# Optimization experiments

Measured on AMD Instinct MI355X. Metric: run time of the kernel, lower is better.

The kernel has to match this reference:

```python
import jax, jax.numpy as jnp
import numpy as np
import math

DIM = 768
HIDDEN = 3072
HEADS = 8
DEPTH = DIM // HEADS
EPS = 1e-5


def gelu_tanh(x):
    c = math.sqrt(2.0 / math.pi)
    return x * 0.5 * (1.0 + jnp.tanh(c * (x + 0.044715 * jnp.power(x, 3))))


def layer_norm(x, g, b):
    mu = jnp.mean(x, axis=-1, keepdims=True)
    var = jnp.mean(jnp.square(x - mu), axis=-1, keepdims=True)
    return (x - mu) * jax.lax.rsqrt(var + EPS) * g + b


def setup_inputs() -> dict:
    key = jax.random.key(0)
    ks = jax.random.split(key, 12)
    B, F, N = 2, 64, 128
    s = 0.02
    return {
        "q": jax.random.normal(ks[0], (B, F, N, DIM), jnp.float32),
        "k": jax.random.normal(ks[1], (B, F, N, DIM), jnp.float32),
        "v": jax.random.normal(ks[2], (B, F, N, DIM), jnp.float32),
        "ln1_g": jnp.ones((DIM,), jnp.float32),
        "ln1_b": jnp.zeros((DIM,), jnp.float32),
        "wq": jax.random.normal(ks[3], (DIM, DIM), jnp.float32) * s,
        "wk": jax.random.normal(ks[4], (DIM, DIM), jnp.float32) * s,
        "wv": jax.random.normal(ks[5], (DIM, DIM), jnp.float32) * s,
        "wo": jax.random.normal(ks[6], (DIM, DIM), jnp.float32) * s,
        "wo_b": jnp.zeros((DIM,), jnp.float32),
        "ln2_g": jnp.ones((DIM,), jnp.float32),
        "ln2_b": jnp.zeros((DIM,), jnp.float32),
        "w1": jax.random.normal(ks[7], (DIM, HIDDEN), jnp.float32) * s,
        "b1": jnp.zeros((HIDDEN,), jnp.float32),
        "w2": jax.random.normal(ks[8], (HIDDEN, DIM), jnp.float32) * s,
        "b2": jnpp if False else jnp.zeros((DIM,), jnp.float32),
    }


def reference(q, k, v, ln1_g, ln1_b, wq, wk, wv, wo, wo_b, ln2_g, ln2_b, w1, b1, w2, b2):
    # Shared norm1 applied to q, k, v (same params, as in the original)
    qn = layer_norm(q, ln1_g, ln1_b)
    kn = layer_norm(k, ln1_g, ln1_b)
    vn = layer_norm(v, ln1_g, ln1_b)

    B, F, N, _ = qn.shape
    # Projections (no bias on wq/wk/wv since att_bias=False)
    def split_heads(x):
        return x.reshape(B, F, N, HEADS, DEPTH).transpose(0, 1, 3, 2, 4)  # b f h n d

    qh = split_heads(qn @ wq)
    kh = split_heads(kn @ wk)
    vh = split_heads(vn @ wv)

    scale = DEPTH ** (-0.5)
    dots = jnp.einsum('bfhid,bfhjd->bfhij', qh, kh) * scale
    att_weight = jax.nn.softmax(dots, axis=-1)
    out = jnp.einsum('bfhij,bfhjd->bfhid', att_weight, vh)
    out = out.transpose(0, 1, 3, 2, 4).reshape(B, F, N, DIM)
    y = out @ wo + wo_b

    y = y + qn  # residual with normed q
    h = gelu_tanh(layer_norm(y, ln2_g, ln2_b) @ w1 + b1)
    out2 = h @ w2 + b2
    return out2 + y, att_weight
```

## Files before the change

kernel.cpp:

```cpp
#include <hip/hip_runtime.h>


#define NROWS 16384
#define TDIM 768
#define THID 3072
#define EPS 1e-5f

typedef short bf16x8 __attribute__((ext_vector_type(8)));
typedef float f32x4 __attribute__((ext_vector_type(4)));

__device__ __forceinline__ float b2f(unsigned short u) {
    union { unsigned int i; float f; } v; v.i = ((unsigned int)u) << 16; return v.f;
}
__device__ __forceinline__ unsigned short f2b(float f) {
    union { float f; unsigned int i; } v; v.f = f;
    unsigned int r = v.i + 0x7fffu + ((v.i >> 16) & 1u);
    return (unsigned short)(r >> 16);
}

__device__ __forceinline__ void async_copy16(const unsigned short* g, unsigned short* l) {
    __builtin_amdgcn_global_load_lds(
        (const __attribute__((address_space(1))) unsigned int*)g,
        (__attribute__((address_space(3))) unsigned int*)l,
        16, 0, 0);
}

__global__ __launch_bounds__(256) void cvt_t_kernel(
    const float* __restrict__ src, unsigned short* __restrict__ dst, int K, int N)
{
    __shared__ unsigned short tile[32][33];
    int n0 = blockIdx.x * 32, k0 = blockIdx.y * 32;
    int tx = threadIdx.x & 31, ty = threadIdx.x >> 5;
#pragma unroll
    for (int r = ty; r < 32; r += 8)
        tile[r][tx] = f2b(src[(size_t)(k0 + r) * N + n0 + tx]);
    __syncthreads();
#pragma unroll
    for (int r = ty; r < 32; r += 8)
        dst[(size_t)(n0 + r) * K + k0 + tx] = tile[tx][r];
}

template<bool IN_F32>
__global__ __launch_bounds__(256) void ln_kernel(
    const void* __restrict__ x0, const void* __restrict__ x1,
    const void* __restrict__ x2,
    const float* __restrict__ g, const float* __restrict__ bb,
    unsigned short* __restrict__ o0, unsigned short* __restrict__ o1,
    unsigned short* __restrict__ o2)
{
    int t = blockIdx.y;
    const void* x = (t == 0) ? x0 : (t == 1) ? x1 : x2;
    unsigned short* o = (t == 0) ? o0 : (t == 1) ? o1 : o2;
    size_t base = (size_t)blockIdx.x * TDIM;
    int tid = threadIdx.x;
    float v[3]; float sum = 0.f, sq = 0.f;
#pragma unroll
    for (int i = 0; i < 3; i++) {
        if constexpr (IN_F32) v[i] = ((const float*)x)[base + tid + i * 256];
        else v[i] = b2f(((const unsigned short*)x)[base + tid + i * 256]);
        sum += v[i]; sq += v[i] * v[i];
    }
#pragma unroll
    for (int o_ = 32; o_ > 0; o_ >>= 1) {
        sum += __shfl_down(sum, o_); sq += __shfl_down(sq, o_);
    }
    __shared__ float s1[4], s2[4];
    __shared__ float smu, srs;
    int wave = tid >> 6, lane = tid & 63;
    if (lane == 0) { s1[wave] = sum; s2[wave] = sq; }
    __syncthreads();
    if (tid == 0) {
        float S = s1[0] + s1[1] + s1[2] + s1[3];
        float Q = s2[0] + s2[1] + s2[2] + s2[3];
        float mu = S / (float)TDIM;
        float var = Q / (float)TDIM - mu * mu;
        smu = mu; srs = rsqrtf(var + EPS);
    }
    __syncthreads();
    float mu = smu, rs = srs;
#pragma unroll
    for (int i = 0; i < 3; i++) {
        int c = tid + i * 256;
        o[base + c] = f2b((v[i] - mu) * rs * g[c] + bb[c]);
    }
}

template<bool BIAS, bool RES, bool GELU, bool OUTF32>
__global__ __launch_bounds__(256) void gemm_kernel(
    const unsigned short* __restrict__ A, const unsigned short* __restrict__ BT,
    const float* __restrict__ bias, const unsigned short* __restrict__ resid,
    void* __restrict__ Cv, int M, int N, int K,
    size_t aStride, size_t bStride, size_t cStride)
{
    __shared__ unsigned short sA[128][32];
    __shared__ unsigned short sB[128][32];
    int tid = threadIdx.x;

    int nbx = gridDim.x;
    int nwg = nbx * gridDim.y;
    int bid = blockIdx.y * nbx + blockIdx.x;
    int xcd = bid & 7, loc = bid >> 3;
    int qc = nwg >> 3, rc = nwg & 7;
    int swz = (xcd < rc ? xcd * (qc + 1) : rc * (qc + 1) + (xcd - rc) * qc) + loc;
    int row0 = (swz / nbx) * 128;
    int col0 = (swz % nbx) * 128;

    int z = blockIdx.z;
    A  += (size_t)z * aStride;
    BT += (size_t)z * bStride;
    size_t zoff = (size_t)z * cStride;

    int wave = tid >> 6, lane = tid & 63;
    int wm = (wave >> 1) * 64, wn = (wave & 1) * 64;
    int cl = lane & 15, quad = lane >> 4;

    f32x4 acc[4][4];
#pragma unroll
    for (int i = 0; i < 4; i++)
#pragma unroll
        for (int j = 0; j < 4; j++) acc[i][j] = (f32x4){0.f, 0.f, 0.f, 0.f};

    const unsigned short* Arow = A + (size_t)row0 * K;
    const unsigned short* Brow = BT + (size_t)col0 * K;

    int c0 = wave * 128 + lane, c1 = c0 + 64;
    const unsigned short* aS0 = Arow + (size_t)(c0 >> 2) * K + ((c0 & 3) << 3);
    const unsigned short* aS1 = Arow + (size_t)(c1 >> 2) * K + ((c1 & 3) << 3);
    const unsigned short* bS0 = Brow + (size_t)(c0 >> 2) * K + ((c0 & 3) << 3);
    const unsigned short* bS1 = Brow + (size_t)(c1 >> 2) * K + ((c1 & 3) << 3);
    unsigned short* aD0 = &sA[0][0] + (size_t)(wave * 128) * 8;
    unsigned short* aD1 = aD0 + 64 * 8;
    unsigned short* bD0 = &sB[0][0] + (size_t)(wave * 128) * 8;
    unsigned short* bD1 = bD0 + 64 * 8;

    for (int k0 = 0; k0 < K; k0 += 32) {
        async_copy16(aS0 + k0, aD0);
        async_copy16(aS1 + k0, aD1);
        async_copy16(bS0 + k0, bD0);
        async_copy16(bS1 + k0, bD1);
        __syncthreads();
        bf16x8 af[4], bfr[4];
#pragma unroll
        for (int mi = 0; mi < 4; mi++)
            af[mi] = *(const bf16x8*)(&sA[wm + mi * 16 + cl][quad * 8]);
#pragma unroll
        for (int ni = 0; ni < 4; ni++)
            bfr[ni] = *(const bf16x8*)(&sB[wn + ni * 16 + cl][quad * 8]);
#pragma unroll
        for (int mi = 0; mi < 4; mi++)
#pragma unroll
            for (int ni = 0; ni < 4; ni++)
                acc[mi][ni] = __builtin_amdgcn_mfma_f32_16x16x32_bf16(
                    af[mi], bfr[ni], acc[mi][ni], 0, 0, 0);
        __syncthreads();
    }

    float bvv[4];
#pragma unroll
    for (int ni = 0; ni < 4; ni++) {
        if constexpr (BIAS) bvv[ni] = bias[col0 + wn + ni * 16 + cl];
        else bvv[ni] = 0.f;
    }
#pragma unroll
    for (int mi = 0; mi < 4; mi++) {
#pragma unroll
        for (int r = 0; r < 4; r++) {
            int gr = row0 + wm + mi * 16 + quad * 4 + r;
            size_t rb = (size_t)gr * N + col0 + wn + cl;
#pragma unroll
            for (int ni = 0; ni < 4; ni++) {
                float v = acc[mi][ni][r];
                if constexpr (BIAS) v += bvv[ni];
                if constexpr (GELU) {
                    float x = v;
                    float t = x + 0.044715f * x * x * x;
                    float e = __expf(-1.5957691216057308f * t);
                    v = x * __builtin_amdgcn_rcpf(1.0f + e);
                }
                if constexpr (RES) v += b2f(resid[rb + ni * 16]);
                size_t idx = rb + ni * 16 + zoff;
                if constexpr (OUTF32) ((float*)Cv)[idx] = v;
                else ((unsigned short*)Cv)[idx] = f2b(v);
            }
        }
    }
}

__global__ __launch_bounds__(256) void attn_fused_kernel(
    const unsigned short* __restrict__ qh, const unsigned short* __restrict__ kh,
    const unsigned short* __restrict__ vh, float* __restrict__ att,
    unsigned short* __restrict__ attout)
{
    __shared__ __align__(16) unsigned short smem[30464];
    __shared__ float wmax[2][128];
    __shared__ float wsum[2][128];
    __shared__ float sInv[128];
    unsigned short* sQ = smem;
    unsigned short* sK = smem + 12288;
    unsigned short* sP = smem;
    unsigned short* sVt = smem + 17408;

    int hb = blockIdx.x, g = hb >> 3, h = hb & 7;
    int tid = threadIdx.x;
    int wave = tid >> 6, lane = tid & 63;
    int cl = lane & 15, quad = lane >> 4;
    int wm = (wave >> 1) * 64, wn = (wave & 1) * 64;

    size_t rbase = (size_t)g * 128 * TDIM + (size_t)h * 96;

#pragma unroll
    for (int it = 0; it < 6; it++) {
        int cb = wave * 384 + it * 64;
        int c = cb + lane;
        int r = c / 12, dc = (c % 12) * 8;
        async_copy16(qh + rbase + (size_t)r * TDIM + dc, sQ + (size_t)cb * 8);
        async_copy16(kh + rbase + (size_t)r * TDIM + dc, sK + (size_t)cb * 8);
    }
    __syncthreads();

    f32x4 acc[4][4];
#pragma unroll
    for (int i = 0; i < 4; i++)
#pragma unroll
        for (int j = 0; j < 4; j++) acc[i][j] = (f32x4){0.f, 0.f, 0.f, 0.f};
#pragma unroll
    for (int kk = 0; kk < 3; kk++) {
        bf16x8 af[4], bfr[4];
#pragma unroll
        for (int mi = 0; mi < 4; mi++)
            af[mi] = *(const bf16x8*)(sQ + (size_t)(wm + mi * 16 + cl) * 96 + kk * 32 + quad * 8);
#pragma unroll
        for (int ni = 0; ni < 4; ni++)
            bfr[ni] = *(const bf16x8*)(sK + (size_t)(wn + ni * 16 + cl) * 96 + kk * 32 + quad * 8);
#pragma unroll
        for (int mi = 0; mi < 4; mi++)
#pragma unroll
            for (int ni = 0; ni < 4; ni++)
                acc[mi][ni] = __builtin_amdgcn_mfma_f32_16x16x32_bf16(
                    af[mi], bfr[ni], acc[mi][ni], 0, 0, 0);
    }

    const float scale = 0.10206207261596575f;
#pragma unroll
    for (int mi = 0; mi < 4; mi++)
#pragma unroll
        for (int ni = 0; ni < 4; ni++)
#pragma unroll
            for (int r = 0; r < 4; r++) acc[mi][ni][r] *= scale;
#pragma unroll
    for (int mi = 0; mi < 4; mi++) {
#pragma unroll
        for (int r = 0; r < 4; r++) {
            float m = fmaxf(fmaxf(acc[mi][0][r], acc[mi][1][r]),
                            fmaxf(acc[mi][2][r], acc[mi][3][r]));
            m = fmaxf(m, __shfl_xor(m, 1));
            m = fmaxf(m, __shfl_xor(m, 2));
            m = fmaxf(m, __shfl_xor(m, 4));
            m = fmaxf(m, __shfl_xor(m, 8));
            if (cl == 0) wmax[wn >> 6][wm + mi * 16 + quad * 4 + r] = m;
        }
    }
    __syncthreads();

    for (int c = tid; c < 1536; c += 256) {
        int kk2 = c / 12, dc2 = (c % 12) * 8;
        uint4 t_ = *(const uint4*)(vh + rbase + (size_t)kk2 * TDIM + dc2);
        unsigned short* tp = (unsigned short*)&t_;
#pragma unroll
        for (int j = 0; j < 8; j++) {
            int jj = (j + tid) & 7;
            sVt[(size_t)(dc2 + jj) * 136 + kk2] = tp[jj];
        }
    }

#pragma unroll
    for (int mi = 0; mi < 4; mi++) {
#pragma unroll
        for (int r = 0; r < 4; r++) {
            int row = wm + mi * 16 + quad * 4 + r;
            float rm = fmaxf(wmax[0][row], wmax[1][row]);
            float s = 0.f;
#pragma unroll
            for (int ni = 0; ni < 4; ni++) {
                float e = __expf(acc[mi][ni][r] - rm);
                acc[mi][ni][r] = e;
                s += e;
            }
            s += __shfl_xor(s, 1);
            s += __shfl_xor(s, 2);
            s += __shfl_xor(s, 4);
            s += __shfl_xor(s, 8);
            if (cl == 0) wsum[wn >> 6][row] = s;
#pragma unroll
            for (int ni = 0; ni < 4; ni++)
                sP[(size_t)row * 136 + wn + ni * 16 + cl] = f2b(acc[mi][ni][r]);
        }
    }
    __syncthreads();

    if (tid < 128) sInv[tid] = 1.0f / (wsum[0][tid] + wsum[1][tid]);
    __syncthreads();

    size_t pbase = (size_t)hb * 128 * 128;
#pragma unroll
    for (int mi = 0; mi < 4; mi++) {
#pragma unroll
        for (int r = 0; r < 4; r++) {
            int row = wm + mi * 16 + quad * 4 + r;
            float iv = sInv[row];
#pragma unroll
            for (int ni = 0; ni < 4; ni++)
                att[pbase + (size_t)row * 128 + wn + ni * 16 + cl] =
                    acc[mi][ni][r] * iv;
        }
    }

    int wm2 = wave * 32;
    f32x4 acc2[2][6];
#pragma unroll
    for (int i = 0; i < 2; i++)
#pragma unroll
        for (int j = 0; j < 6; j++) acc2[i][j] = (f32x4){0.f, 0.f, 0.f, 0.f};
#pragma unroll
    for (int ks = 0; ks < 4; ks++) {
        bf16x8 pa[2], vb[6];
#pragma unroll
        for (int mi2 = 0; mi2 < 2; mi2++)
            pa[mi2] = *(const bf16x8*)(sP + (size_t)(wm2 + mi2 * 16 + cl) * 136 + ks * 32 + quad * 8);
#pragma unroll
        for (int ni2 = 0; ni2 < 6; ni2++)
            vb[ni2] = *(const bf16x8*)(sVt + (size_t)(ni2 * 16 + cl) * 136 + ks * 32 + quad * 8);
#pragma unroll
        for (int mi2 = 0; mi2 < 2; mi2++)
#pragma unroll
            for (int ni2 = 0; ni2 < 6; ni2++)
                acc2[mi2][ni2] = __builtin_amdgcn_mfma_f32_16x16x32_bf16(
                    pa[mi2], vb[ni2], acc2[mi2][ni2], 0, 0, 0);
    }
#pragma unroll
    for (int mi2 = 0; mi2 < 2; mi2++) {
#pragma unroll
        for (int r = 0; r < 4; r++) {
            int row = wm2 + mi2 * 16 + quad * 4 + r;
            float iv = sInv[row];
#pragma unroll
            for (int ni2 = 0; ni2 < 6; ni2++) {
                int d = ni2 * 16 + cl;
                attout[rbase + (size_t)row * TDIM + d] =
                    f2b(acc2[mi2][ni2][r] * iv);
            }
        }
    }
}

extern "C" void kernel_launch(void* const* d_in, const int* in_sizes, int n_in,
                              void* d_out, int out_size, void* d_ws, size_t ws_size,
                              hipStream_t stream)
{
    const float* q     = (const float*)d_in[0];
    const float* k     = (const float*)d_in[1];
    const float* v     = (const float*)d_in[2];
    const float* ln1_g = (const float*)d_in[3];
    const float* ln1_b = (const float*)d_in[4];
    const float* wq    = (const float*)d_in[5];
    const float* wk    = (const float*)d_in[6];
    const float* wv    = (const float*)d_in[7];
    const float* wo    = (const float*)d_in[8];
    const float* wo_b  = (const float*)d_in[9];
    const float* ln2_g = (const float*)d_in[10];
    const float* ln2_b = (const float*)d_in[11];
    const float* w1    = (const float*)d_in[12];
    const float* b1    = (const float*)d_in[13];
    const float* w2    = (const float*)d_in[14];
    const float* b2    = (const float*)d_in[15];

    float* out0 = (float*)d_out;
    const size_t S = (size_t)NROWS * TDIM;
    float* att = out0 + S;
    unsigned short* ws = (unsigned short*)d_ws;
    if (ws_size < 7 * S * sizeof(unsigned short)) return;

    const size_t W = (size_t)TDIM * TDIM;
    const size_t W2 = (size_t)TDIM * THID;

    unsigned short* qn     = ws;
    unsigned short* kn     = ws + S;
    unsigned short* vn     = ws + 2 * S;
    unsigned short* qh     = ws + 3 * S;
    unsigned short* wqkvoT = ws + 6 * S;
    unsigned short* attout = ws + S;
    unsigned short* y      = ws + 2 * S;
    unsigned short* ln2y   = ws;
    unsigned short* w1T    = ws + S;
    unsigned short* w2T    = ws + S + W2;
    unsigned short* hbuf   = ws + 3 * S;

    dim3 blk(256);
    cvt_t_kernel<<<dim3(24, 24), blk, 0, stream>>>(wq, wqkvoT + 0 * W, TDIM, TDIM);
    cvt_t_kernel<<<dim3(24, 24), blk, 0, stream>>>(wk, wqkvoT + 1 * W, TDIM, TDIM);
    cvt_t_kernel<<<dim3(24, 24), blk, 0, stream>>>(wv, wqkvoT + 2 * W, TDIM, TDIM);
    cvt_t_kernel<<<dim3(24, 24), blk, 0, stream>>>(wo, wqkvoT + 3 * W, TDIM, TDIM);
    ln_kernel<true><<<dim3(NROWS, 3), blk, 0, stream>>>(
        q, k, v, ln1_g, ln1_b, qn, kn, vn);
    gemm_kernel<false, false, false, false><<<dim3(6, 128, 3), blk, 0, stream>>>(
        qn, wqkvoT, nullptr, nullptr, qh, NROWS, TDIM, TDIM, S, W, S);
    attn_fused_kernel<<<dim3(1024), blk, 0, stream>>>(qh, qh + S, qh + 2 * S, att, attout);
    gemm_kernel<true, true, false, false><<<dim3(6, 128), blk, 0, stream>>>(
        attout, wqkvoT + 3 * W, wo_b, qn, y, NROWS, TDIM, TDIM, 0, 0, 0);
    cvt_t_kernel<<<dim3(96, 24), blk, 0, stream>>>(w1, w1T, TDIM, THID);
    cvt_t_kernel<<<dim3(24, 96), blk, 0, stream>>>(w2, w2T, THID, TDIM);
    ln_kernel<false><<<dim3(NROWS, 1), blk, 0, stream>>>(
        y, y, y, ln2_g, ln2_b, ln2y, ln2y, ln2y);
    gemm_kernel<true, false, true, false><<<dim3(24, 128), blk, 0, stream>>>(
        ln2y, w1T, b1, nullptr, hbuf, NROWS, THID, TDIM, 0, 0, 0);
    gemm_kernel<true, true, false, true><<<dim3(6, 128), blk, 0, stream>>>(
        hbuf, w2T, b2, y, out0, NROWS, TDIM, THID, 0, 0, 0);
}
```

Baseline: 702.2 us.

## Add 256x256-tile GEMM with XCD swizzle for the FFN up-projection

Adds a new 512-thread GEMM kernel with 256x256 output tiles, double-buffered async global-to-LDS loads, a swizzled LDS layout and an XCD-aware block remapping, and uses it for the w1 GEMM with bias and GELU fused in. The larger tile raises arithmetic intensity and operand reuse per LDS load compared with the previous 128-size tiles. The cost is heavy register use (128 accumulator floats per thread), which lowers occupancy, and fewer workgroups (768), which could hurt load balance.

```diff
diff --git a/kernel.cpp b/kernel.cpp
--- a/kernel.cpp
+++ b/kernel.cpp
@@ -181,6 +181,121 @@
                 size_t idx = rb + ni * 16 + zoff;
                 if constexpr (OUTF32) ((float*)Cv)[idx] = v;
                 else ((unsigned short*)Cv)[idx] = f2b(v);
+            }
+        }
+    }
+}
+
+template<bool BIAS, bool GELU>
+__global__ __launch_bounds__(512) void gemm256_kernel(
+    const unsigned short* __restrict__ A, const unsigned short* __restrict__ BT,
+    const float* __restrict__ bias, unsigned short* __restrict__ C,
+    int N, int K)
+{
+    __shared__ unsigned short sA[2][256][32];
+    __shared__ unsigned short sB[2][256][32];
+    int tid = threadIdx.x;
+
+    int nbx = gridDim.x;
+    int nwg = nbx * gridDim.y;
+    int bid = blockIdx.y * nbx + blockIdx.x;
+    int xcd = bid & 7, loc = bid >> 3;
+    int qc = nwg >> 3, rc = nwg & 7;
+    int swz = (xcd < rc ? xcd * (qc + 1) : rc * (qc + 1) + (xcd - rc) * qc) + loc;
+    int row0 = (swz / nbx) * 256;
+    int col0 = (swz % nbx) * 256;
+
+    int wave = tid >> 6, lane = tid & 63;
+    int wr = wave >> 2, wc = wave & 3;
+    int cl = lane & 15, quad = lane >> 4;
+    int sl8 = (quad ^ ((cl >> 1) & 3)) << 3;
+
+    size_t rowoff = (size_t)(tid >> 2) * K + (size_t)(((tid & 3) ^ ((tid >> 3) & 3)) << 3);
+    const unsigned short* aS0 = A + (size_t)row0 * K + rowoff;
+    const unsigned short* aS1 = aS0 + (size_t)128 * K;
+    const unsigned short* bS0 = BT + (size_t)col0 * K + rowoff;
+    const unsigned short* bS1 = bS0 + (size_t)128 * K;
+    unsigned short* aD = &sA[0][0][0] + (wave * 64) * 8;
+    unsigned short* bD = &sB[0][0][0] + (wave * 64) * 8;
+
+    f32x4 acc[8][4];
+#pragma unroll
+    for (int i = 0; i < 8; i++)
+#pragma unroll
+        for (int j = 0; j < 4; j++) acc[i][j] = (f32x4){0.f, 0.f, 0.f, 0.f};
+
+    int NT = K >> 5;
+    async_copy16(aS0, aD);
+    async_copy16(aS1, aD + 4096);
+    async_copy16(bS0, bD);
+    async_copy16(bS1, bD + 4096);
+
+    for (int t = 0; t < NT; ++t) {
+        int cur = t & 1;
+        if (t + 1 < NT) {
+            int nb = (cur ^ 1) * 8192;
+            int ko = (t + 1) << 5;
+            async_copy16(aS0 + ko, aD + nb);
+            async_copy16(aS1 + ko, aD + nb + 4096);
+            async_copy16(bS0 + ko, bD + nb);
+            async_copy16(bS1 + ko, bD + nb + 4096);
+            asm volatile("s_waitcnt vmcnt(4)" ::: "memory");
+        } else {
+            asm volatile("s_waitcnt vmcnt(0)" ::: "memory");
+        }
+        __builtin_amdgcn_s_barrier();
+        __builtin_amdgcn_sched_barrier(0);
+        const unsigned short* pA = &sA[cur][0][0];
+        const unsigned short* pB = &sB[cur][0][0];
+        bf16x8 bfr[4], af[4];
+#pragma unroll
+        for (int ni = 0; ni < 4; ni++)
+            bfr[ni] = *(const bf16x8*)(pB + (wc * 64 + ni * 16 + cl) * 32 + sl8);
+#pragma unroll
+        for (int mi = 0; mi < 4; mi++)
+            af[mi] = *(const bf16x8*)(pA + (wr * 128 + mi * 16 + cl) * 32 + sl8);
+#pragma unroll
+        for (int mi = 0; mi < 4; mi++)
+#pragma unroll
+            for (int ni = 0; ni < 4; ni++)
+                acc[mi][ni] = __builtin_amdgcn_mfma_f32_16x16x32_bf16(
+                    af[mi], bfr[ni], acc[mi][ni], 0, 0, 0);
+#pragma unroll
+        for (int mi = 0; mi < 4; mi++)
+            af[mi] = *(const bf16x8*)(pA + (wr * 128 + 64 + mi * 16 + cl) * 32 + sl8);
+#pragma unroll
+        for (int mi = 0; mi < 4; mi++)
+#pragma unroll
+            for (int ni = 0; ni < 4; ni++)
+                acc[mi + 4][ni] = __builtin_amdgcn_mfma_f32_16x16x32_bf16(
+                    af[mi], bfr[ni], acc[mi + 4][ni], 0, 0, 0);
+        __builtin_amdgcn_sched_barrier(0);
+        __builtin_amdgcn_s_barrier();
+        __builtin_amdgcn_sched_barrier(0);
+    }
+
+    float bvv[4];
+#pragma unroll
+    for (int ni = 0; ni < 4; ni++) {
+        if constexpr (BIAS) bvv[ni] = bias[col0 + wc * 64 + ni * 16 + cl];
+        else bvv[ni] = 0.f;
+    }
+#pragma unroll
+    for (int mi = 0; mi < 8; mi++) {
+#pragma unroll
+        for (int r = 0; r < 4; r++) {
+            int gr = row0 + wr * 128 + mi * 16 + quad * 4 + r;
+            size_t rb = (size_t)gr * N + col0 + wc * 64 + cl;
+#pragma unroll
+            for (int ni = 0; ni < 4; ni++) {
+                float v = acc[mi][ni][r] + bvv[ni];
+                if constexpr (GELU) {
+                    float x = v;
+                    float tt = x + 0.044715f * x * x * x;
+                    float e = __expf(-1.5957691216057308f * tt);
+                    v = x * __builtin_amdgcn_rcpf(1.0f + e);
+                }
+                C[rb + ni * 16] = f2b(v);
             }
         }
     }
@@ -411,8 +526,8 @@
     cvt_t_kernel<<<dim3(24, 96), blk, 0, stream>>>(w2, w2T, THID, TDIM);
     ln_kernel<false><<<dim3(NROWS, 1), blk, 0, stream>>>(
         y, y, y, ln2_g, ln2_b, ln2y, ln2y, ln2y);
-    gemm_kernel<true, false, true, false><<<dim3(24, 128), blk, 0, stream>>>(
-        ln2y, w1T, b1, nullptr, hbuf, NROWS, THID, TDIM, 0, 0, 0);
+    gemm256_kernel<true, true><<<dim3(12, 64), dim3(512), 0, stream>>>(
+        ln2y, w1T, b1, hbuf, THID, TDIM);
     gemm_kernel<true, true, false, true><<<dim3(6, 128), blk, 0, stream>>>(
         hbuf, w2T, b2, y, out0, NROWS, TDIM, THID, 0, 0, 0);
 }
```

After: 691.4 us. Within noise of the previous version (-1.5%).
